# Kernel tuning notes

Hardware: AMD Instinct MI355X
Metric: run time of the kernel (lower is better)

Reference implementation:

```python
import jax, jax.numpy as jnp
import numpy as np

HARMONICS = 5


def _harmonic_basis(x):
    k = jnp.arange(1, HARMONICS + 1, dtype=x.dtype)            # [H]
    kx = x[..., None] * k                                       # [B, D, H]
    sc = jnp.stack([jnp.sin(kx), jnp.cos(kx)], axis=-1)         # [B, D, H, 2]
    sc = sc.reshape(*x.shape, 2 * HARMONICS)                    # interleaved sin/cos
    ones = jnp.ones((*x.shape, 1), dtype=x.dtype)
    return jnp.concatenate([ones, sc], axis=-1)                 # [B, D, 2H+1]


def setup_inputs() -> dict:
    key = jax.random.key(0)
    k1, k2, k3 = jax.random.split(key, 3)
    B, D, F, H = 16384, 256, 11, 256
    x = jax.random.normal(k1, (B, D), dtype=jnp.float32)
    W = jax.random.normal(k2, (D, F, H), dtype=jnp.float32) * (1.0 / np.sqrt(F))
    b = jax.random.normal(k3, (D, H), dtype=jnp.float32) * 0.01
    return {"x": x, "W": W, "b": b}


def reference(x, W, b) -> jnp.ndarray:
    # basis expansion per feature, batched small GEMM, summed over features
    basis = _harmonic_basis(x)                                  # [B, D, F]
    out = jnp.einsum('bdf,dfh->bh', basis, W)                   # sum over features fused
    out = out + jnp.sum(b, axis=0)                              # sum of per-feature biases
    return out
```

## Files before the change

kernel.cpp:

```cpp
#include <hip/hip_runtime.h>
#include <hip/hip_bf16.h>


#define BDIM 16384
#define DDIM 256
#define HOUT 256
#define NKT  80
#define BM 64
#define BN 128

typedef __bf16 bf16x8 __attribute__((ext_vector_type(8)));
typedef float floatx4 __attribute__((ext_vector_type(4)));

__device__ __forceinline__ unsigned short f2bf(float f) {
    unsigned int u = __float_as_uint(f);
    return (unsigned short)((u + 0x7FFFu + ((u >> 16) & 1u)) >> 16);
}

__device__ __forceinline__ unsigned int pkbf(float a, float b) {
    __hip_bfloat162 r = __float22bfloat162_rn(make_float2(a, b));
    return *reinterpret_cast<unsigned int*>(&r);
}

__global__ void prep_kernel(const float* __restrict__ W, const float* __restrict__ bias,
                            unsigned short* __restrict__ Wfrag, float* __restrict__ c_part) {
    const int bid = blockIdx.x;
    const int t = threadIdx.x;
    if (bid < 4 * NKT) {
        const int kt = bid >> 2;
        const int sub = bid & 3;
        const int dtile = kt / 10;
        const int f = kt - dtile * 10 + 1;
        const int d0 = dtile * 32 + sub * 8;
        const float* wsrc = W + ((size_t)d0 * 11 + f) * 256 + t;
        union { unsigned short s[8]; int4 v; } buf;
#pragma unroll
        for (int dd = 0; dd < 8; ++dd)
            buf.s[dd] = f2bf(wsrc[(size_t)dd * 11 * 256]);
        *(int4*)(Wfrag + ((size_t)kt * 256 + t) * 32 + sub * 8) = buf.v;
    } else {
        const int p = bid - 4 * NKT;
        float acc = 0.f;
#pragma unroll
        for (int dd = 0; dd < 32; ++dd) {
            const int d = p * 32 + dd;
            acc += W[(size_t)(d * 11) * 256 + t] + bias[(size_t)d * 256 + t];
        }
        c_part[p * 256 + t] = acc;
    }
}

__device__ __forceinline__ void stage_phase(const unsigned short* __restrict__ Wfrag,
                                            unsigned short* lbuf, int kt0,
                                            int h0, int wave, int l15, int koff) {
#pragma unroll
    for (int s = 0; s < 10; ++s) {
        const int c = wave * 10 + s;
        const int ktl = c >> 3;
        const int f = c & 7;
        const unsigned short* g = Wfrag + (size_t)(kt0 + ktl) * 8192
                                + (h0 + f * 16 + l15) * 32 + koff * 8;
        __builtin_amdgcn_global_load_lds((const void*)g, (void*)(lbuf + c * 512), 16, 0, 0);
    }
}

__global__ __launch_bounds__(256, 2)
void kan_gemm(const float* __restrict__ x, const unsigned short* __restrict__ Wfrag,
              const float* __restrict__ c_part, float* __restrict__ out) {
    __shared__ unsigned short Bs[2][5 * 8 * 512];

    const int t = threadIdx.x;
    const int m0 = blockIdx.x * BM;
    const int h0 = blockIdx.y * BN;

    const int lane = t & 63;
    const int wave = t >> 6;
    const int wr = wave >> 1;
    const int wc = wave & 1;
    const int l15 = lane & 15;
    const int koff = lane >> 4;

    floatx4 acc[2][4];
#pragma unroll
    for (int i = 0; i < 2; ++i)
#pragma unroll
        for (int j = 0; j < 4; ++j)
            acc[i][j] = (floatx4){0.f, 0.f, 0.f, 0.f};

    const float* xr0 = x + (size_t)(m0 + wr * 32 + l15) * DDIM + koff * 8;

    float4 xn[4];
    xn[0] = *(const float4*)(xr0 + 0);
    xn[1] = *(const float4*)(xr0 + 4);
    xn[2] = *(const float4*)(xr0 + 16 * DDIM + 0);
    xn[3] = *(const float4*)(xr0 + 16 * DDIM + 4);

    stage_phase(Wfrag, &Bs[0][0], 0, h0, wave, l15, koff);
    __syncthreads();

    float sc[16], cc[16], sp[16], cp[16], t2c[16];

#pragma unroll
    for (int p = 0; p < 16; ++p) {
        const int dt = p >> 1;
        const int half = p & 1;
        const int buf = p & 1;

        if (p < 15)
            stage_phase(Wfrag, &Bs[buf ^ 1][0], (p + 1) * 5, h0, wave, l15, koff);

        if (half == 0) {
#pragma unroll
            for (int i = 0; i < 2; ++i)
#pragma unroll
                for (int e = 0; e < 8; ++e) {
                    const int g = i * 8 + e;
                    const float xv = ((const float*)&xn[i * 2 + (e >> 2)])[e & 3];
                    __sincosf(xv, &sc[g], &cc[g]);
                    t2c[g] = cc[g] + cc[g];
                    sp[g] = 0.f;
                    cp[g] = 1.f;
                }
        }

#pragma unroll
        for (int kl = 0; kl < 5; ++kl) {
            const int hs = half * 5 + kl;
            const float* src = (hs & 1) ? cc : sc;

            union { unsigned int u[4]; bf16x8 v; } a0, a1;
#pragma unroll
            for (int q = 0; q < 4; ++q) {
                a0.u[q] = pkbf(src[2 * q], src[2 * q + 1]);
                a1.u[q] = pkbf(src[8 + 2 * q], src[8 + 2 * q + 1]);
            }

            const unsigned short* fb = &Bs[buf][(kl * 8 + wc * 4) * 512 + lane * 8];
            const bf16x8 b0 = *(const bf16x8*)(fb);
            const bf16x8 b1 = *(const bf16x8*)(fb + 512);
            const bf16x8 b2 = *(const bf16x8*)(fb + 1024);
            const bf16x8 b3 = *(const bf16x8*)(fb + 1536);

            acc[0][0] = __builtin_amdgcn_mfma_f32_16x16x32_bf16(a0.v, b0, acc[0][0], 0, 0, 0);
            acc[1][0] = __builtin_amdgcn_mfma_f32_16x16x32_bf16(a1.v, b0, acc[1][0], 0, 0, 0);
            acc[0][1] = __builtin_amdgcn_mfma_f32_16x16x32_bf16(a0.v, b1, acc[0][1], 0, 0, 0);
            acc[1][1] = __builtin_amdgcn_mfma_f32_16x16x32_bf16(a1.v, b1, acc[1][1], 0, 0, 0);
            acc[0][2] = __builtin_amdgcn_mfma_f32_16x16x32_bf16(a0.v, b2, acc[0][2], 0, 0, 0);
            acc[1][2] = __builtin_amdgcn_mfma_f32_16x16x32_bf16(a1.v, b2, acc[1][2], 0, 0, 0);
            acc[0][3] = __builtin_amdgcn_mfma_f32_16x16x32_bf16(a0.v, b3, acc[0][3], 0, 0, 0);
            acc[1][3] = __builtin_amdgcn_mfma_f32_16x16x32_bf16(a1.v, b3, acc[1][3], 0, 0, 0);

            if ((hs & 1) && hs < 9) {
#pragma unroll
                for (int g = 0; g < 16; ++g) {
                    const float ns = t2c[g] * sc[g] - sp[g];
                    const float nc = t2c[g] * cc[g] - cp[g];
                    sp[g] = sc[g]; cp[g] = cc[g];
                    sc[g] = ns;   cc[g] = nc;
                }
            }
        }

        if (half == 1 && dt < 7) {
            xn[0] = *(const float4*)(xr0 + (dt + 1) * 32 + 0);
            xn[1] = *(const float4*)(xr0 + (dt + 1) * 32 + 4);
            xn[2] = *(const float4*)(xr0 + 16 * DDIM + (dt + 1) * 32 + 0);
            xn[3] = *(const float4*)(xr0 + 16 * DDIM + (dt + 1) * 32 + 4);
        }

        __syncthreads();
    }

    float cj[4];
#pragma unroll
    for (int j = 0; j < 4; ++j) {
        const int col = h0 + wc * 64 + j * 16 + l15;
        float s = 0.f;
#pragma unroll
        for (int q = 0; q < 8; ++q) s += c_part[q * 256 + col];
        cj[j] = s;
    }
#pragma unroll
    for (int i = 0; i < 2; ++i) {
        const int row0 = m0 + wr * 32 + i * 16 + koff * 4;
#pragma unroll
        for (int j = 0; j < 4; ++j) {
            const int col = h0 + wc * 64 + j * 16 + l15;
#pragma unroll
            for (int r = 0; r < 4; ++r)
                out[(size_t)(row0 + r) * HOUT + col] = acc[i][j][r] + cj[j];
        }
    }
}

extern "C" void kernel_launch(void* const* d_in, const int* in_sizes, int n_in,
                              void* d_out, int out_size, void* d_ws, size_t ws_size,
                              hipStream_t stream) {
    const float* x = (const float*)d_in[0];
    const float* W = (const float*)d_in[1];
    const float* b = (const float*)d_in[2];
    float* out = (float*)d_out;

    unsigned short* Wfrag = (unsigned short*)d_ws;
    float* c_part = (float*)((char*)d_ws + (size_t)NKT * 256 * 32 * 2);

    prep_kernel<<<4 * NKT + 8, 256, 0, stream>>>(W, b, Wfrag, c_part);
    kan_gemm<<<dim3(BDIM / BM, HOUT / BN), 256, 0, stream>>>(x, Wfrag, c_part, out);
}
```

Before: 106.9 us.

## Split K across two wave groups with LDS reduction in GEMM kernel

Doubles the block to 512 threads. The two halves of the waves each process half of the D features (split-K), with finer pipeline phases of two k-tiles per stage. At the end the second group writes its partial accumulators to LDS and the first group adds them before storing. This aims to raise wave occupancy and hide latency of the sin/cos recurrence and MFMA chains. The cost is an extra LDS reduction, more barriers, and higher register pressure under the new launch bounds.

Measured after the change: 210.3 us. +96.8%, slower.

```diff
diff --git a/kernel.cpp b/kernel.cpp
--- a/kernel.cpp
+++ b/kernel.cpp
@@ -51,23 +51,25 @@
 }
 
 __device__ __forceinline__ void stage_phase(const unsigned short* __restrict__ Wfrag,
-                                            unsigned short* lbuf, int kt0,
+                                            unsigned short* lbuf, int ph,
                                             int h0, int wave, int l15, int koff) {
 #pragma unroll
-    for (int s = 0; s < 10; ++s) {
-        const int c = wave * 10 + s;
-        const int ktl = c >> 3;
+    for (int s = 0; s < 4; ++s) {
+        const int c = wave * 4 + s;
+        const int kh_c = c >> 4;
+        const int ktl = (c >> 3) & 1;
         const int f = c & 7;
-        const unsigned short* g = Wfrag + (size_t)(kt0 + ktl) * 8192
+        const int ktg = kh_c * 40 + ph * 2 + ktl;
+        const unsigned short* g = Wfrag + (size_t)ktg * 8192
                                 + (h0 + f * 16 + l15) * 32 + koff * 8;
         __builtin_amdgcn_global_load_lds((const void*)g, (void*)(lbuf + c * 512), 16, 0, 0);
     }
 }
 
-__global__ __launch_bounds__(256, 2)
+__global__ __launch_bounds__(512, 4)
 void kan_gemm(const float* __restrict__ x, const unsigned short* __restrict__ Wfrag,
               const float* __restrict__ c_part, float* __restrict__ out) {
-    __shared__ unsigned short Bs[2][5 * 8 * 512];
+    __shared__ unsigned short Bs[2][4 * 8 * 512];
 
     const int t = threadIdx.x;
     const int m0 = blockIdx.x * BM;
@@ -75,8 +77,10 @@
 
     const int lane = t & 63;
     const int wave = t >> 6;
-    const int wr = wave >> 1;
-    const int wc = wave & 1;
+    const int kh = wave >> 2;
+    const int wq = wave & 3;
+    const int wr = wq >> 1;
+    const int wc = wq & 1;
     const int l15 = lane & 15;
     const int koff = lane >> 4;
 
@@ -87,7 +91,7 @@
         for (int j = 0; j < 4; ++j)
             acc[i][j] = (floatx4){0.f, 0.f, 0.f, 0.f};
 
-    const float* xr0 = x + (size_t)(m0 + wr * 32 + l15) * DDIM + koff * 8;
+    const float* xr0 = x + (size_t)(m0 + wr * 32 + l15) * DDIM + koff * 8 + kh * 128;
 
     float4 xn[4];
     xn[0] = *(const float4*)(xr0 + 0);
@@ -101,15 +105,13 @@
     float sc[16], cc[16], sp[16], cp[16], t2c[16];
 
 #pragma unroll
-    for (int p = 0; p < 16; ++p) {
-        const int dt = p >> 1;
-        const int half = p & 1;
-        const int buf = p & 1;
-
-        if (p < 15)
-            stage_phase(Wfrag, &Bs[buf ^ 1][0], (p + 1) * 5, h0, wave, l15, koff);
-
-        if (half == 0) {
+    for (int ph = 0; ph < 20; ++ph) {
+        const int buf = ph & 1;
+
+        if (ph < 19)
+            stage_phase(Wfrag, &Bs[buf ^ 1][0], ph + 1, h0, wave, l15, koff);
+
+        if (ph % 5 == 0) {
 #pragma unroll
             for (int i = 0; i < 2; ++i)
 #pragma unroll
@@ -124,8 +126,8 @@
         }
 
 #pragma unroll
-        for (int kl = 0; kl < 5; ++kl) {
-            const int hs = half * 5 + kl;
+        for (int s = 0; s < 2; ++s) {
+            const int hs = (ph * 2 + s) % 10;
             const float* src = (hs & 1) ? cc : sc;
 
             union { unsigned int u[4]; bf16x8 v; } a0, a1;
@@ -135,7 +137,7 @@
                 a1.u[q] = pkbf(src[8 + 2 * q], src[8 + 2 * q + 1]);
             }
 
-            const unsigned short* fb = &Bs[buf][(kl * 8 + wc * 4) * 512 + lane * 8];
+            const unsigned short* fb = &Bs[buf][((kh * 2 + s) * 8 + wc * 4) * 512 + lane * 8];
             const bf16x8 b0 = *(const bf16x8*)(fb);
             const bf16x8 b1 = *(const bf16x8*)(fb + 512);
             const bf16x8 b2 = *(const bf16x8*)(fb + 1024);
@@ -161,34 +163,48 @@
             }
         }
 
-        if (half == 1 && dt < 7) {
-            xn[0] = *(const float4*)(xr0 + (dt + 1) * 32 + 0);
-            xn[1] = *(const float4*)(xr0 + (dt + 1) * 32 + 4);
-            xn[2] = *(const float4*)(xr0 + 16 * DDIM + (dt + 1) * 32 + 0);
-            xn[3] = *(const float4*)(xr0 + 16 * DDIM + (dt + 1) * 32 + 4);
+        if (ph % 5 == 2 && ph < 15) {
+            const int dn = ph / 5 + 1;
+            xn[0] = *(const float4*)(xr0 + dn * 32 + 0);
+            xn[1] = *(const float4*)(xr0 + dn * 32 + 4);
+            xn[2] = *(const float4*)(xr0 + 16 * DDIM + dn * 32 + 0);
+            xn[3] = *(const float4*)(xr0 + 16 * DDIM + dn * 32 + 4);
         }
 
         __syncthreads();
     }
 
-    float cj[4];
-#pragma unroll
-    for (int j = 0; j < 4; ++j) {
-        const int col = h0 + wc * 64 + j * 16 + l15;
-        float s = 0.f;
-#pragma unroll
-        for (int q = 0; q < 8; ++q) s += c_part[q * 256 + col];
-        cj[j] = s;
-    }
-#pragma unroll
-    for (int i = 0; i < 2; ++i) {
-        const int row0 = m0 + wr * 32 + i * 16 + koff * 4;
+    float* red = (float*)&Bs[0][0];
+    if (kh == 1) {
+#pragma unroll
+        for (int i = 0; i < 2; ++i)
+#pragma unroll
+            for (int j = 0; j < 4; ++j)
+                *(floatx4*)&red[(((wq * 2 + i) * 4 + j) * 256) + lane * 4] = acc[i][j];
+    }
+    __syncthreads();
+
+    if (kh == 0) {
+        float cj[4];
 #pragma unroll
         for (int j = 0; j < 4; ++j) {
             const int col = h0 + wc * 64 + j * 16 + l15;
-#pragma unroll
-            for (int r = 0; r < 4; ++r)
-                out[(size_t)(row0 + r) * HOUT + col] = acc[i][j][r] + cj[j];
+            float s = 0.f;
+#pragma unroll
+            for (int q = 0; q < 8; ++q) s += c_part[q * 256 + col];
+            cj[j] = s;
+        }
+#pragma unroll
+        for (int i = 0; i < 2; ++i) {
+            const int row0 = m0 + wr * 32 + i * 16 + koff * 4;
+#pragma unroll
+            for (int j = 0; j < 4; ++j) {
+                const int col = h0 + wc * 64 + j * 16 + l15;
+                const floatx4 v = *(const floatx4*)&red[(((wq * 2 + i) * 4 + j) * 256) + lane * 4];
+#pragma unroll
+                for (int r = 0; r < 4; ++r)
+                    out[(size_t)(row0 + r) * HOUT + col] = acc[i][j][r] + v[r] + cj[j];
+            }
         }
     }
 }
@@ -205,5 +221,5 @@
     float* c_part = (float*)((char*)d_ws + (size_t)NKT * 256 * 32 * 2);
 
     prep_kernel<<<4 * NKT + 8, 256, 0, stream>>>(W, b, Wfrag, c_part);
-    kan_gemm<<<dim3(BDIM / BM, HOUT / BN), 256, 0, stream>>>(x, Wfrag, c_part, out);
-}
+    kan_gemm<<<dim3(BDIM / BM, HOUT / BN), 512, 0, stream>>>(x, Wfrag, c_part, out);
+}
```

## Replace two-stage LDS double buffer with five-slot ring and vmcnt-based waits

Applied to the files above, without the earlier changes.

The weight-staging pipeline moves from two large LDS buffers, each holding five k-tiles, to a five-slot ring of two-tile stages kept three stages ahead. Each stage now waits with s_waitcnt vmcnt plus a single raw s_barrier, instead of a full __syncthreads after every half-tile. The aim is to keep more global-to-LDS loads in flight and cut barrier stall time. The x prefetch is dropped and x is loaded at the start of each d-tile. That load latency can now be exposed, and the outer loop is no longer unrolled.

Measured after the change: 107.1 us. About the same (+0.2%).

```diff
diff --git a/kernel.cpp b/kernel.cpp
--- a/kernel.cpp
+++ b/kernel.cpp
@@ -51,14 +51,14 @@
 }
 
 __device__ __forceinline__ void stage_phase(const unsigned short* __restrict__ Wfrag,
-                                            unsigned short* lbuf, int kt0,
+                                            unsigned short* lbuf, int ph,
                                             int h0, int wave, int l15, int koff) {
 #pragma unroll
-    for (int s = 0; s < 10; ++s) {
-        const int c = wave * 10 + s;
+    for (int s = 0; s < 4; ++s) {
+        const int c = wave * 4 + s;
         const int ktl = c >> 3;
         const int f = c & 7;
-        const unsigned short* g = Wfrag + (size_t)(kt0 + ktl) * 8192
+        const unsigned short* g = Wfrag + (size_t)(ph * 2 + ktl) * 8192
                                 + (h0 + f * 16 + l15) * 32 + koff * 8;
         __builtin_amdgcn_global_load_lds((const void*)g, (void*)(lbuf + c * 512), 16, 0, 0);
     }
@@ -67,7 +67,7 @@
 __global__ __launch_bounds__(256, 2)
 void kan_gemm(const float* __restrict__ x, const unsigned short* __restrict__ Wfrag,
               const float* __restrict__ c_part, float* __restrict__ out) {
-    __shared__ unsigned short Bs[2][5 * 8 * 512];
+    __shared__ unsigned short Bs[5][2 * 8 * 512];
 
     const int t = threadIdx.x;
     const int m0 = blockIdx.x * BM;
@@ -89,87 +89,84 @@
 
     const float* xr0 = x + (size_t)(m0 + wr * 32 + l15) * DDIM + koff * 8;
 
-    float4 xn[4];
-    xn[0] = *(const float4*)(xr0 + 0);
-    xn[1] = *(const float4*)(xr0 + 4);
-    xn[2] = *(const float4*)(xr0 + 16 * DDIM + 0);
-    xn[3] = *(const float4*)(xr0 + 16 * DDIM + 4);
-
     stage_phase(Wfrag, &Bs[0][0], 0, h0, wave, l15, koff);
-    __syncthreads();
+    stage_phase(Wfrag, &Bs[1][0], 1, h0, wave, l15, koff);
+    stage_phase(Wfrag, &Bs[2][0], 2, h0, wave, l15, koff);
 
     float sc[16], cc[16], sp[16], cp[16], t2c[16];
 
-#pragma unroll
-    for (int p = 0; p < 16; ++p) {
-        const int dt = p >> 1;
-        const int half = p & 1;
-        const int buf = p & 1;
-
-        if (p < 15)
-            stage_phase(Wfrag, &Bs[buf ^ 1][0], (p + 1) * 5, h0, wave, l15, koff);
-
-        if (half == 0) {
-#pragma unroll
-            for (int i = 0; i < 2; ++i)
-#pragma unroll
-                for (int e = 0; e < 8; ++e) {
-                    const int g = i * 8 + e;
-                    const float xv = ((const float*)&xn[i * 2 + (e >> 2)])[e & 3];
-                    __sincosf(xv, &sc[g], &cc[g]);
+#pragma unroll 1
+    for (int dt = 0; dt < 8; ++dt) {
+        const float4 xa0 = *(const float4*)(xr0 + dt * 32 + 0);
+        const float4 xb0 = *(const float4*)(xr0 + dt * 32 + 4);
+        const float4 xa1 = *(const float4*)(xr0 + 16 * DDIM + dt * 32 + 0);
+        const float4 xb1 = *(const float4*)(xr0 + 16 * DDIM + dt * 32 + 4);
+
+#pragma unroll
+        for (int q = 0; q < 5; ++q) {
+            {
+                int pt = dt * 5 + q + 3;
+                if (pt > 39) pt = 39;
+                stage_phase(Wfrag, &Bs[(q + 3) % 5][0], pt, h0, wave, l15, koff);
+            }
+
+            __builtin_amdgcn_sched_barrier(0);
+            asm volatile("s_waitcnt vmcnt(8)" ::: "memory");
+            __builtin_amdgcn_s_barrier();
+            __builtin_amdgcn_sched_barrier(0);
+
+            if (q == 0) {
+                const float xv[16] = {xa0.x, xa0.y, xa0.z, xa0.w, xb0.x, xb0.y, xb0.z, xb0.w,
+                                      xa1.x, xa1.y, xa1.z, xa1.w, xb1.x, xb1.y, xb1.z, xb1.w};
+#pragma unroll
+                for (int g = 0; g < 16; ++g) {
+                    __sincosf(xv[g], &sc[g], &cc[g]);
                     t2c[g] = cc[g] + cc[g];
                     sp[g] = 0.f;
                     cp[g] = 1.f;
                 }
-        }
-
-#pragma unroll
-        for (int kl = 0; kl < 5; ++kl) {
-            const int hs = half * 5 + kl;
-            const float* src = (hs & 1) ? cc : sc;
-
-            union { unsigned int u[4]; bf16x8 v; } a0, a1;
-#pragma unroll
-            for (int q = 0; q < 4; ++q) {
-                a0.u[q] = pkbf(src[2 * q], src[2 * q + 1]);
-                a1.u[q] = pkbf(src[8 + 2 * q], src[8 + 2 * q + 1]);
             }
 
-            const unsigned short* fb = &Bs[buf][(kl * 8 + wc * 4) * 512 + lane * 8];
-            const bf16x8 b0 = *(const bf16x8*)(fb);
-            const bf16x8 b1 = *(const bf16x8*)(fb + 512);
-            const bf16x8 b2 = *(const bf16x8*)(fb + 1024);
-            const bf16x8 b3 = *(const bf16x8*)(fb + 1536);
-
-            acc[0][0] = __builtin_amdgcn_mfma_f32_16x16x32_bf16(a0.v, b0, acc[0][0], 0, 0, 0);
-            acc[1][0] = __builtin_amdgcn_mfma_f32_16x16x32_bf16(a1.v, b0, acc[1][0], 0, 0, 0);
-            acc[0][1] = __builtin_amdgcn_mfma_f32_16x16x32_bf16(a0.v, b1, acc[0][1], 0, 0, 0);
-            acc[1][1] = __builtin_amdgcn_mfma_f32_16x16x32_bf16(a1.v, b1, acc[1][1], 0, 0, 0);
-            acc[0][2] = __builtin_amdgcn_mfma_f32_16x16x32_bf16(a0.v, b2, acc[0][2], 0, 0, 0);
-            acc[1][2] = __builtin_amdgcn_mfma_f32_16x16x32_bf16(a1.v, b2, acc[1][2], 0, 0, 0);
-            acc[0][3] = __builtin_amdgcn_mfma_f32_16x16x32_bf16(a0.v, b3, acc[0][3], 0, 0, 0);
-            acc[1][3] = __builtin_amdgcn_mfma_f32_16x16x32_bf16(a1.v, b3, acc[1][3], 0, 0, 0);
-
-            if ((hs & 1) && hs < 9) {
-#pragma unroll
-                for (int g = 0; g < 16; ++g) {
-                    const float ns = t2c[g] * sc[g] - sp[g];
-                    const float nc = t2c[g] * cc[g] - cp[g];
-                    sp[g] = sc[g]; cp[g] = cc[g];
-                    sc[g] = ns;   cc[g] = nc;
+#pragma unroll
+            for (int s = 0; s < 2; ++s) {
+                const float* src = s ? cc : sc;
+
+                union { unsigned int u[4]; bf16x8 v; } a0, a1;
+#pragma unroll
+                for (int p = 0; p < 4; ++p) {
+                    a0.u[p] = pkbf(src[2 * p], src[2 * p + 1]);
+                    a1.u[p] = pkbf(src[8 + 2 * p], src[8 + 2 * p + 1]);
+                }
+
+                const unsigned short* fb = &Bs[q][(s * 8 + wc * 4) * 512 + lane * 8];
+                const bf16x8 b0 = *(const bf16x8*)(fb);
+                const bf16x8 b1 = *(const bf16x8*)(fb + 512);
+                const bf16x8 b2 = *(const bf16x8*)(fb + 1024);
+                const bf16x8 b3 = *(const bf16x8*)(fb + 1536);
+
+                acc[0][0] = __builtin_amdgcn_mfma_f32_16x16x32_bf16(a0.v, b0, acc[0][0], 0, 0, 0);
+                acc[1][0] = __builtin_amdgcn_mfma_f32_16x16x32_bf16(a1.v, b0, acc[1][0], 0, 0, 0);
+                acc[0][1] = __builtin_amdgcn_mfma_f32_16x16x32_bf16(a0.v, b1, acc[0][1], 0, 0, 0);
+                acc[1][1] = __builtin_amdgcn_mfma_f32_16x16x32_bf16(a1.v, b1, acc[1][1], 0, 0, 0);
+                acc[0][2] = __builtin_amdgcn_mfma_f32_16x16x32_bf16(a0.v, b2, acc[0][2], 0, 0, 0);
+                acc[1][2] = __builtin_amdgcn_mfma_f32_16x16x32_bf16(a1.v, b2, acc[1][2], 0, 0, 0);
+                acc[0][3] = __builtin_amdgcn_mfma_f32_16x16x32_bf16(a0.v, b3, acc[0][3], 0, 0, 0);
+                acc[1][3] = __builtin_amdgcn_mfma_f32_16x16x32_bf16(a1.v, b3, acc[1][3], 0, 0, 0);
+
+                if (s == 1 && q < 4) {
+#pragma unroll
+                    for (int g = 0; g < 16; ++g) {
+                        const float ns = t2c[g] * sc[g] - sp[g];
+                        const float nc = t2c[g] * cc[g] - cp[g];
+                        sp[g] = sc[g]; cp[g] = cc[g];
+                        sc[g] = ns;   cc[g] = nc;
+                    }
                 }
             }
         }
-
-        if (half == 1 && dt < 7) {
-            xn[0] = *(const float4*)(xr0 + (dt + 1) * 32 + 0);
-            xn[1] = *(const float4*)(xr0 + (dt + 1) * 32 + 4);
-            xn[2] = *(const float4*)(xr0 + 16 * DDIM + (dt + 1) * 32 + 0);
-            xn[3] = *(const float4*)(xr0 + 16 * DDIM + (dt + 1) * 32 + 4);
-        }
-
-        __syncthreads();
-    }
+    }
+
+    asm volatile("s_waitcnt vmcnt(0)" ::: "memory");
 
     float cj[4];
 #pragma unroll
```
